# Performance work log

Hardware: AMD Instinct MI355X
Metric: run time of the kernel (lower is better)

Reference implementation:

```python
import jax, jax.numpy as jnp
import numpy as np

B, S, D, H = 512, 200, 512, 8
FF = 1024          # dim_feedforward == hidden_dim
EMB, HID, FIN = 128, 1024, 64
V = 100000
QK_SCALE, ATTN_CLIP, FFN_CLIP, QKV_CLIP = 0.05, 3.0, 2.0, 1.0
PAD = 0


def _ln(x, g, b, eps=1e-6):
    m = jnp.mean(x, -1, keepdims=True)
    v = jnp.mean((x - m) ** 2, -1, keepdims=True)
    return (x - m) / jnp.sqrt(v + eps) * g + b


def setup_inputs() -> dict:
    key = jax.random.key(0)
    ks = jax.random.split(key, 32)
    n = lambda i, shape, s=0.02: (s * jax.random.normal(ks[i], shape)).astype(jnp.float32)
    emb_table = n(0, (V, D)).at[PAD].set(0.0)  # padding row zeroed
    inp = {
        'item_seq': jax.random.randint(ks[20], (B, S), 0, V),
        'user_avg_ctr': jax.random.uniform(ks[21], (B,)),
        'user_total_interactions': jax.random.uniform(ks[22], (B,)),
        'age_price': jax.random.randint(ks[23], (B,), 0, 100),
        'gender_cate': jax.random.randint(ks[24], (B,), 0, 10),
        'cms_group_id': jax.random.randint(ks[25], (B,), 0, 13),
        'emb_table': emb_table,
        'in_proj_w': n(1, (3 * D, D)),
        'out_proj_w': n(2, (D, D)),
        'out_proj_b': jnp.zeros((D,), jnp.float32),
        'ln1_g': jnp.ones((D,), jnp.float32), 'ln1_b': jnp.zeros((D,), jnp.float32),
        'ln2_g': jnp.ones((D,), jnp.float32), 'ln2_b': jnp.zeros((D,), jnp.float32),
        'lin1_w': n(3, (FF, D)), 'lin1_b': jnp.zeros((FF,), jnp.float32),
        'lin2_w': n(4, (D, FF)), 'lin2_b': jnp.zeros((D,), jnp.float32),
        'age_tab': n(5, (100, EMB)), 'gender_tab': n(6, (10, EMB)), 'cms_tab': n(7, (13, EMB)),
        'ctr_w': n(8, (EMB, 1)), 'ctr_b': jnp.zeros((EMB,), jnp.float32),
        'ti_w': n(9, (EMB, 1)), 'ti_b': jnp.zeros((EMB,), jnp.float32),
        'mlp1_w': n(10, (HID, D + 5 * EMB)), 'mlp1_b': jnp.zeros((HID,), jnp.float32),
        'mlp2_w': n(11, (FIN, HID)), 'mlp2_b': jnp.zeros((FIN,), jnp.float32),
    }
    return inp


def reference(item_seq, user_avg_ctr, user_total_interactions, age_price, gender_cate,
              cms_group_id, emb_table, in_proj_w, out_proj_w, out_proj_b,
              ln1_g, ln1_b, ln2_g, ln2_b, lin1_w, lin1_b, lin2_w, lin2_b,
              age_tab, gender_tab, cms_tab, ctr_w, ctr_b, ti_w, ti_b,
              mlp1_w, mlp1_b, mlp2_w, mlp2_b):
    dk = D // H
    pad = item_seq == PAD  # [B,S] key padding mask
    x = jnp.clip(emb_table[item_seq] * 0.5, -1.0, 1.0)  # [B,S,D]

    # ---- custom self-attention block (no in_proj bias, heavy clamping) ----
    qw, kw, vw = in_proj_w[:D], in_proj_w[D:2 * D], in_proj_w[2 * D:]
    q = jnp.clip(x @ qw.T, -QKV_CLIP, QKV_CLIP)
    k = jnp.clip(x @ kw.T, -QKV_CLIP, QKV_CLIP)
    v = jnp.clip(x @ vw.T, -QKV_CLIP, QKV_CLIP)
    q = q.reshape(B, S, H, dk).transpose(0, 2, 1, 3)
    k = k.reshape(B, S, H, dk).transpose(0, 2, 1, 3)
    v = v.reshape(B, S, H, dk).transpose(0, 2, 1, 3)
    scores = jnp.einsum('bhqd,bhkd->bhqk', q, k) / (np.float32(np.sqrt(dk)) * QK_SCALE)
    scores = jnp.clip(scores, -ATTN_CLIP, ATTN_CLIP)
    scores = jnp.where(pad[:, None, None, :], -1e9, scores)
    w = jax.nn.softmax(scores, axis=-1)  # dropout is identity in eval
    x2 = jnp.einsum('bhqk,bhkd->bhqd', w, v).transpose(0, 2, 1, 3).reshape(B, S, D)
    x2 = jnp.clip(x2 @ out_proj_w.T + out_proj_b, -ATTN_CLIP, ATTN_CLIP)
    sa = _ln(x + x2, ln1_g, ln1_b)          # norm1 inside overridden _sa_block
    x = _ln(x + sa, ln1_g, ln1_b)           # base post-norm wraps norm1 again

    # ---- FFN block with clamps ----
    h = jax.nn.relu(jnp.clip(x @ lin1_w.T + lin1_b, -FFN_CLIP, FFN_CLIP))
    f2 = jnp.clip(h @ lin2_w.T + lin2_b, -FFN_CLIP, FFN_CLIP)
    ff = _ln(x + f2, ln2_g, ln2_b)          # norm2 inside overridden _ff_block
    x = _ln(x + ff, ln2_g, ln2_b)           # base wraps norm2 again

    seq_out = jnp.clip(x, -5.0, 5.0)
    m = (~pad).astype(seq_out.dtype)[:, :, None]
    seq_rep = jnp.clip((seq_out * m).sum(1) / (m.sum(1) + 1e-8), -5.0, 5.0)  # [B,D]

    ape = age_tab[age_price]
    ge = gender_tab[gender_cate]
    ce = cms_tab[cms_group_id]
    ctr = user_avg_ctr[:, None] @ ctr_w.T + ctr_b
    ti = user_total_interactions[:, None] @ ti_w.T + ti_b
    u = jnp.concatenate([seq_rep, ctr, ti, ape, ge, ce], axis=-1)  # [B, D+5*EMB]
    return jax.nn.relu(u @ mlp1_w.T + mlp1_b) @ mlp2_w.T + mlp2_b  # [B, FIN]
```

## Files before the change

kernel.cpp:

```cpp
#include <hip/hip_runtime.h>
#include <hip/hip_bf16.h>
#include <stdint.h>

typedef __attribute__((ext_vector_type(8))) short short8;
typedef __attribute__((ext_vector_type(4))) float f32x4;
typedef unsigned short u16;

#define MFMA16(a,b,c) __builtin_amdgcn_mfma_f32_16x16x32_bf16((a),(b),(c),0,0,0)

__device__ __forceinline__ u16 f2bf(float f) {
  unsigned int u = __float_as_uint(f);
  return (u16)((u + 0x7FFFu + ((u >> 16) & 1u)) >> 16);
}
__device__ __forceinline__ float bf2f(u16 h) {
  return __uint_as_float(((unsigned int)h) << 16);
}
__device__ __forceinline__ float clampf(float v, float lo, float hi) {
  return fminf(fmaxf(v, lo), hi);
}
__device__ __forceinline__ void gl2lds16(const u16* g, u16* l) {
  __builtin_amdgcn_global_load_lds(
      (const __attribute__((address_space(1))) unsigned int*)g,
      (__attribute__((address_space(3))) unsigned int*)(uintptr_t)l,
      16, 0, 0);
}

__global__ __launch_bounds__(256) void cvt_bf16_kernel(
    const float* __restrict__ src, u16* __restrict__ dst, int n) {
  for (int i = blockIdx.x*256 + threadIdx.x; i < n; i += gridDim.x*256)
    dst[i] = f2bf(src[i]);
}

__global__ __launch_bounds__(256) void embed_kernel(
    const int* __restrict__ iseq, const float* __restrict__ emb,
    u16* __restrict__ xb) {
  int gid = blockIdx.x*256 + threadIdx.x;
  int m = gid >> 7;
  int c = (gid & 127) * 4;
  int item = iseq[m];
  float4 e = *(const float4*)&emb[(size_t)item*512 + c];
  ushort4 hb;
  hb.x = f2bf(clampf(e.x*0.5f, -1.f, 1.f));
  hb.y = f2bf(clampf(e.y*0.5f, -1.f, 1.f));
  hb.z = f2bf(clampf(e.z*0.5f, -1.f, 1.f));
  hb.w = f2bf(clampf(e.w*0.5f, -1.f, 1.f));
  *(ushort4*)&xb[(size_t)m*512 + c] = hb;
}

__global__ __launch_bounds__(256) void cnt_kernel(
    const int* __restrict__ item_seq, float* __restrict__ cnt) {
  __shared__ int sred[4];
  int b = blockIdx.x, tid = threadIdx.x;
  int lane = tid & 63, wv = tid >> 6;
  int c = 0;
  if (tid < 200) c = (item_seq[b*200 + tid] != 0) ? 1 : 0;
  #pragma unroll
  for (int m = 1; m <= 32; m <<= 1) c += __shfl_xor(c, m);
  if (lane == 0) sred[wv] = c;
  __syncthreads();
  if (tid == 0) cnt[b] = (float)(sred[0]+sred[1]+sred[2]+sred[3]);
}

#define BAR() asm volatile("s_barrier" ::: "memory")
#define LGKM0() do { asm volatile("s_waitcnt lgkmcnt(0)" ::: "memory"); \
                     __builtin_amdgcn_sched_barrier(0); } while (0)
#define VM4() asm volatile("s_waitcnt vmcnt(4)" ::: "memory")
#define VM0() asm volatile("s_waitcnt vmcnt(0)" ::: "memory")

__device__ __forceinline__ void stage_half(const char* gsrc0, size_t rstride,
                                           u16* lhalf, int wv, int lane) {
  #pragma unroll
  for (int j = 0; j < 2; ++j) {
    const int o   = j*8192 + wv*1024 + lane*16;
    const int row = o >> 7;
    const int cb  = (o & 127) ^ ((row & 7) << 4);
    gl2lds16((const u16*)(gsrc0 + (size_t)row*rstride + cb),
             (u16*)((char*)lhalf + j*8192 + wv*1024));
  }
}

__device__ __forceinline__ short8 ldsfrag(const u16* slot, int row, int kb) {
  return *(const short8*)((const char*)slot + row*128 + (kb ^ ((row & 7) << 4)));
}

#define QUAD(AH, NB)                                                          \
  _Pragma("unroll")                                                           \
  for (int i = 0; i < 4; ++i)                                                 \
    _Pragma("unroll")                                                         \
    for (int nf = 0; nf < 2; ++nf)                                            \
      _Pragma("unroll")                                                       \
      for (int ks = 0; ks < 2; ++ks)                                          \
        acc[(AH)*4 + i][(NB)*2 + nf] =                                        \
            MFMA16(af[AH][i][ks], bf[nf][ks], acc[(AH)*4 + i][(NB)*2 + nf]);

#define RD_AF(H, SLOT)                                                        \
  _Pragma("unroll")                                                           \
  for (int i = 0; i < 4; ++i)                                                 \
    _Pragma("unroll")                                                         \
    for (int ks = 0; ks < 2; ++ks)                                            \
      af[H][i][ks] = ldsfrag((SLOT), wm*128 + (H)*64 + i*16 + r16, ks*64 + q4*16);

#define RD_BF(SLOT, OFF)                                                      \
  _Pragma("unroll")                                                           \
  for (int nf = 0; nf < 2; ++nf)                                              \
    _Pragma("unroll")                                                         \
    for (int ks = 0; ks < 2; ++ks)                                            \
      bf[nf][ks] = ldsfrag((SLOT), wn*64 + (OFF) + nf*16 + r16, ks*64 + q4*16);

template <int MODE>
__global__ __launch_bounds__(512, 2)
void gemm_bt(const u16* __restrict__ A, const u16* __restrict__ Bw,
             const float* __restrict__ bias, int K, int Nt, int swz,
             u16* __restrict__ outB, u16* __restrict__ QKV, long long projStride) {
  __shared__ __align__(16) u16 SH[65536];
  u16* const As0 = SH;
  u16* const As1 = SH + 16384;
  u16* const Bs0 = SH + 32768;
  u16* const Bs1 = SH + 49152;
  const int tid  = threadIdx.x;
  const int lane = tid & 63;
  const int wv   = tid >> 6;
  const int wm   = wv >> 2;
  const int wn   = wv & 3;
  const int id   = blockIdx.x;
  int mt, nt2;
  if (swz) { mt = (id / (8*Nt))*8 + (id & 7); nt2 = (id >> 3) % Nt; }
  else     { mt = id / Nt;                    nt2 = id % Nt; }
  const int m0 = mt * 256;
  const int n0 = nt2 * 256;
  const int KT = K >> 6;
  const int NI = KT >> 1;

  const char* Abase = (const char*)(A  + (size_t)m0*K);
  const char* Bbase = (const char*)(Bw + (size_t)n0*K);
  const size_t rs = (size_t)K * 2;

  const int r16 = lane & 15;
  const int q4  = lane >> 4;

  const f32x4 fz = {0.f, 0.f, 0.f, 0.f};
  f32x4 acc[8][4];
  #pragma unroll
  for (int i = 0; i < 8; ++i)
    #pragma unroll
    for (int j = 0; j < 4; ++j) acc[i][j] = fz;

  short8 af[2][4][2];
  short8 bf[2][2];

  stage_half(Abase,              rs, As0,             wv, lane);
  stage_half(Abase + 128*rs,     rs, As0 + 128*64,    wv, lane);
  stage_half(Bbase,              rs, Bs0,             wv, lane);
  stage_half(Bbase + 128*rs,     rs, Bs0 + 128*64,    wv, lane);
  stage_half(Abase + 128,        rs, As1,             wv, lane);
  stage_half(Abase + 128*rs + 128, rs, As1 + 128*64,  wv, lane);
  VM4();
  BAR();

  for (int it = 0; it < NI; ++it) {
    const int ta = it*2;
    const bool m2 = (ta + 2 < KT);
    const char* gBb  = Bbase + (size_t)(ta+1)*128;
    const char* gAa2 = Abase + (size_t)(ta+2)*128;
    const char* gBa2 = Bbase + (size_t)(ta+2)*128;
    const char* gAb1 = Abase + (size_t)(ta+3)*128;

    RD_AF(0, As0); RD_BF(Bs0, 0);
    asm volatile("s_waitcnt lgkmcnt(8)" ::: "memory");
    stage_half(gBb, rs, Bs1, wv, lane);
    BAR(); LGKM0();
    __builtin_amdgcn_s_setprio(1); QUAD(0, 0); __builtin_amdgcn_s_setprio(0);
    VM4(); BAR();

    RD_AF(1, As0);
    stage_half(gBb + 128*rs, rs, Bs1 + 128*64, wv, lane);
    BAR(); LGKM0();
    __builtin_amdgcn_s_setprio(1); QUAD(1, 0); __builtin_amdgcn_s_setprio(0);
    VM4(); BAR();

    RD_BF(Bs0, 32);
    if (m2) stage_half(gAa2, rs, As0, wv, lane);
    BAR(); LGKM0();
    __builtin_amdgcn_s_setprio(1); QUAD(1, 1); __builtin_amdgcn_s_setprio(0);
    VM4(); BAR();

    if (m2) stage_half(gAa2 + 128*rs, rs, As0 + 128*64, wv, lane);
    BAR();
    __builtin_amdgcn_s_setprio(1); QUAD(0, 1); __builtin_amdgcn_s_setprio(0);
    if (m2) { VM4(); } else { VM0(); }
    BAR();

    RD_AF(0, As1); RD_BF(Bs1, 0);
    asm volatile("s_waitcnt lgkmcnt(8)" ::: "memory");
    if (m2) stage_half(gBa2, rs, Bs0, wv, lane);
    BAR(); LGKM0();
    __builtin_amdgcn_s_setprio(1); QUAD(0, 0); __builtin_amdgcn_s_setprio(0);
    VM4(); BAR();

    RD_AF(1, As1);
    if (m2) stage_half(gBa2 + 128*rs, rs, Bs0 + 128*64, wv, lane);
    BAR(); LGKM0();
    __builtin_amdgcn_s_setprio(1); QUAD(1, 0); __builtin_amdgcn_s_setprio(0);
    VM4(); BAR();

    RD_BF(Bs1, 32);
    if (m2) stage_half(gAb1, rs, As1, wv, lane);
    BAR(); LGKM0();
    __builtin_amdgcn_s_setprio(1); QUAD(1, 1); __builtin_amdgcn_s_setprio(0);
    VM4(); BAR();

    if (m2) stage_half(gAb1 + 128*rs, rs, As1 + 128*64, wv, lane);
    BAR();
    __builtin_amdgcn_s_setprio(1); QUAD(0, 1); __builtin_amdgcn_s_setprio(0);
    VM4(); BAR();
  }

  {
    u16* const L = SH;
    const int LROW = 272;
    #pragma unroll
    for (int h = 0; h < 2; ++h) {
      if (h == 1) __syncthreads();
      if (wm == h) {
        #pragma unroll
        for (int nf = 0; nf < 4; ++nf) {
          const int col_l = wn*64 + nf*16 + r16;
          const float bvs = (MODE == 0) ? 0.f : bias[n0 + col_l];
          #pragma unroll
          for (int mi = 0; mi < 8; ++mi) {
            const int row_l = mi*16 + q4*4;
            #pragma unroll
            for (int r = 0; r < 4; ++r) {
              float v = acc[mi][nf][r];
              if (MODE == 0)      v = clampf(v, -1.f, 1.f);
              else if (MODE == 1) v = clampf(v + bvs, -3.f, 3.f);
              else if (MODE == 2) v = fmaxf(clampf(v + bvs, -2.f, 2.f), 0.f);
              else                v = clampf(v + bvs, -2.f, 2.f);
              L[(row_l + r)*LROW + col_l] = f2bf(v);
            }
          }
        }
      }
      __syncthreads();
      #pragma unroll
      for (int k = 0; k < 8; ++k) {
        const int ch   = wv*512 + k*64 + lane;
        const int row  = ch >> 5;
        const int colu = (ch & 31) * 8;
        short8 d = *(const short8*)&L[row*LROW + colu];
        const int rowg = m0 + h*128 + row;
        const int cg   = n0 + colu;
        if (MODE == 0) {
          const unsigned proj = (unsigned)cg >> 9;
          const unsigned hh   = ((unsigned)cg >> 6) & 7u;
          const unsigned dk   = (unsigned)cg & 63u;
          const int b = rowg / 200;
          const int s = rowg - b*200;
          *(short8*)&QKV[(size_t)proj*projStride + (size_t)hh*12800
                         + (size_t)b*102400 + (size_t)s*64 + dk] = d;
        } else {
          const int N = (MODE == 2) ? 1024 : 512;
          *(short8*)&outB[(size_t)rowg*N + cg] = d;
        }
      }
    }
  }
}

__global__ __launch_bounds__(512)
void attn_kernel(const u16* __restrict__ Q, const u16* __restrict__ K,
                 const u16* __restrict__ V, const int* __restrict__ iseq,
                 u16* __restrict__ x2b) {
  __shared__ __align__(16) u16 Ks[208*72];
  __shared__ __align__(16) u16 Vs[64*232];
  __shared__ __align__(16) u16 Ps[8][16*40];
  __shared__ float msk[208];

  const int tid = threadIdx.x, lane = tid & 63, wv = tid >> 6;
  const unsigned bid = blockIdx.x;
  const int h = bid & 7;
  const int b = bid >> 3;
  const size_t bh = (size_t)b*8 + h;
  const u16* Kg = K + bh*12800;
  const u16* Vg = V + bh*12800;
  const u16* Qg = Q + bh*12800;

  for (int c = tid; c < 3200; c += 512) {
    int row = c >> 4, q = c & 15;
    *(ushort4*)&Ks[row*72 + q*4] = *(const ushort4*)&Kg[row*64 + q*4];
  }
  {
    const int quad = wv*2 + (lane >> 5);
    const int sl   = lane & 31;
    #pragma unroll
    for (int it = 0; it < 7; ++it) {
      const int s = sl + it*32;
      if (s < 200) {
        ushort4 v4 = *(const ushort4*)&Vg[s*64 + quad*4];
        Vs[(quad*4+0)*232 + s] = v4.x;
        Vs[(quad*4+1)*232 + s] = v4.y;
        Vs[(quad*4+2)*232 + s] = v4.z;
        Vs[(quad*4+3)*232 + s] = v4.w;
      }
    }
  }
  for (int c = tid; c < 2048; c += 512) {
    int dk = c >> 5, s2 = 200 + (c & 31);
    Vs[dk*232 + s2] = 0;
  }
  for (int t = tid; t < 208; t += 512)
    msk[t] = (t < 200 && iseq[b*200 + t] != 0) ? 1.f : 0.f;
  __syncthreads();

  const int colk = lane & 15;
  const int fk8 = (lane >> 4) * 8;
  const int prow = (lane >> 4) * 4;
  const f32x4 fz = {0.f,0.f,0.f,0.f};

  for (int qb = 0; qb < 2; ++qb) {
    const int qrow = qb*128 + wv*16 + (lane & 15);
    const int qsrc = qrow < 200 ? qrow : 199;
    short8 qa0 = *(const short8*)&Qg[(size_t)qsrc*64 + fk8];
    short8 qa1 = *(const short8*)&Qg[(size_t)qsrc*64 + 32 + fk8];
    f32x4 oacc[4];
    #pragma unroll
    for (int nt = 0; nt < 4; ++nt) oacc[nt] = fz;
    float rs[4] = {0.f,0.f,0.f,0.f};

    for (int kt2 = 0; kt2 < 7; ++kt2) {
      #pragma unroll
      for (int half = 0; half < 2; ++half) {
        const int stile = kt2*2 + half;
        if (stile < 13) {
          const int key = stile*16 + colk;
          short8 kb0 = *(const short8*)&Ks[key*72 + fk8];
          short8 kb1 = *(const short8*)&Ks[key*72 + 32 + fk8];
          f32x4 sc = fz;
          __builtin_amdgcn_s_setprio(1);
          sc = MFMA16(qa0, kb0, sc);
          sc = MFMA16(qa1, kb1, sc);
          __builtin_amdgcn_s_setprio(0);
          const float mk = msk[key];
          #pragma unroll
          for (int r = 0; r < 4; ++r) {
            float p = __expf(clampf(sc[r]*2.5f, -3.f, 3.f)) * mk;
            rs[r] += p;
            Ps[wv][(prow + r)*40 + half*16 + colk] = f2bf(p);
          }
        } else {
          #pragma unroll
          for (int r = 0; r < 4; ++r)
            Ps[wv][(prow + r)*40 + half*16 + colk] = 0;
        }
      }
      asm volatile("s_waitcnt lgkmcnt(0)" ::: "memory");
      short8 pa = *(const short8*)&Ps[wv][(lane & 15)*40 + fk8];
      const int kb32 = kt2*32;
      __builtin_amdgcn_s_setprio(1);
      #pragma unroll
      for (int nt = 0; nt < 4; ++nt) {
        short8 vb = *(const short8*)&Vs[(nt*16 + colk)*232 + kb32 + fk8];
        oacc[nt] = MFMA16(pa, vb, oacc[nt]);
      }
      __builtin_amdgcn_s_setprio(0);
      asm volatile("s_waitcnt lgkmcnt(0)" ::: "memory");
    }

    #pragma unroll
    for (int m = 1; m <= 8; m <<= 1)
      #pragma unroll
      for (int r = 0; r < 4; ++r) rs[r] += __shfl_xor(rs[r], m);

    const int srow = qb*128 + wv*16 + prow;
    #pragma unroll
    for (int r = 0; r < 4; ++r) {
      const int s = srow + r;
      if (s < 200) {
        const float inv = rs[r] > 0.f ? 1.f/rs[r] : 0.f;
        const size_t base = ((size_t)b*200 + s)*512 + h*64;
        #pragma unroll
        for (int nt = 0; nt < 4; ++nt)
          x2b[base + nt*16 + colk] = f2bf(oacc[nt][r] * inv);
      }
    }
  }
}

__global__ __launch_bounds__(256)
void ln1_kernel(const u16* __restrict__ xb, const u16* __restrict__ x2b,
                const float* __restrict__ g, const float* __restrict__ bb,
                u16* __restrict__ xnb) {
  const int lane = threadIdx.x & 63, wv = threadIdx.x >> 6;
  const size_t t = (size_t)blockIdx.x*4 + wv;
  const int c0 = lane*4, c1 = 256 + lane*4;
  ushort4 xa = *(const ushort4*)&xb[t*512 + c0];
  ushort4 xc = *(const ushort4*)&xb[t*512 + c1];
  ushort4 ha = *(const ushort4*)&x2b[t*512 + c0];
  ushort4 hc = *(const ushort4*)&x2b[t*512 + c1];
  float xv[8] = {bf2f(xa.x),bf2f(xa.y),bf2f(xa.z),bf2f(xa.w),
                 bf2f(xc.x),bf2f(xc.y),bf2f(xc.z),bf2f(xc.w)};
  float tv[8] = {xv[0]+bf2f(ha.x), xv[1]+bf2f(ha.y), xv[2]+bf2f(ha.z), xv[3]+bf2f(ha.w),
                 xv[4]+bf2f(hc.x), xv[5]+bf2f(hc.y), xv[6]+bf2f(hc.z), xv[7]+bf2f(hc.w)};
  float s1 = 0.f, s2 = 0.f;
  #pragma unroll
  for (int i = 0; i < 8; ++i) { s1 += tv[i]; s2 += tv[i]*tv[i]; }
  #pragma unroll
  for (int m = 1; m <= 32; m <<= 1) { s1 += __shfl_xor(s1, m); s2 += __shfl_xor(s2, m); }
  float mean = s1*(1.f/512.f);
  float inv = 1.f/sqrtf(s2*(1.f/512.f) - mean*mean + 1e-6f);
  float4 ga = *(const float4*)(g + c0), gc = *(const float4*)(g + c1);
  float4 ba = *(const float4*)(bb + c0), bc = *(const float4*)(bb + c1);
  float gv[8] = {ga.x,ga.y,ga.z,ga.w, gc.x,gc.y,gc.z,gc.w};
  float bv[8] = {ba.x,ba.y,ba.z,ba.w, bc.x,bc.y,bc.z,bc.w};
  float uv[8]; float s3 = 0.f, s4 = 0.f;
  #pragma unroll
  for (int i = 0; i < 8; ++i) {
    float sa = (tv[i]-mean)*inv*gv[i] + bv[i];
    uv[i] = xv[i] + sa;
    s3 += uv[i]; s4 += uv[i]*uv[i];
  }
  #pragma unroll
  for (int m = 1; m <= 32; m <<= 1) { s3 += __shfl_xor(s3, m); s4 += __shfl_xor(s4, m); }
  float mean2 = s3*(1.f/512.f);
  float inv2 = 1.f/sqrtf(s4*(1.f/512.f) - mean2*mean2 + 1e-6f);
  ushort4 o0, o1;
  o0.x = f2bf((uv[0]-mean2)*inv2*gv[0] + bv[0]);
  o0.y = f2bf((uv[1]-mean2)*inv2*gv[1] + bv[1]);
  o0.z = f2bf((uv[2]-mean2)*inv2*gv[2] + bv[2]);
  o0.w = f2bf((uv[3]-mean2)*inv2*gv[3] + bv[3]);
  o1.x = f2bf((uv[4]-mean2)*inv2*gv[4] + bv[4]);
  o1.y = f2bf((uv[5]-mean2)*inv2*gv[5] + bv[5]);
  o1.z = f2bf((uv[6]-mean2)*inv2*gv[6] + bv[6]);
  o1.w = f2bf((uv[7]-mean2)*inv2*gv[7] + bv[7]);
  *(ushort4*)&xnb[t*512 + c0] = o0;
  *(ushort4*)&xnb[t*512 + c1] = o1;
}

__global__ __launch_bounds__(256)
void ln2_kernel(const u16* __restrict__ xnb, const u16* __restrict__ f2b,
                const float* __restrict__ g, const float* __restrict__ bb,
                const int* __restrict__ iseq, float* __restrict__ seq_acc) {
  const int tid = threadIdx.x, lane = tid & 63, wv = tid >> 6;
  const int q = blockIdx.x, bl = blockIdx.y;
  const int c8 = lane*8;
  float gv[8], bv[8];
  *(float4*)&gv[0] = *(const float4*)(g + c8);
  *(float4*)&gv[4] = *(const float4*)(g + c8 + 4);
  *(float4*)&bv[0] = *(const float4*)(bb + c8);
  *(float4*)&bv[4] = *(const float4*)(bb + c8 + 4);
  float acc[8] = {};
  for (int i = wv; i < 50; i += 4) {
    const int s = q*50 + i;
    const size_t row = (size_t)bl*200 + s;
    short8 xh = *(const short8*)&xnb[row*512 + c8];
    short8 yh = *(const short8*)&f2b[row*512 + c8];
    float xv[8], tv[8];
    #pragma unroll
    for (int j = 0; j < 8; ++j) {
      xv[j] = bf2f((u16)xh[j]);
      tv[j] = xv[j] + bf2f((u16)yh[j]);
    }
    float s1 = 0.f, s2 = 0.f;
    #pragma unroll
    for (int j = 0; j < 8; ++j) { s1 += tv[j]; s2 += tv[j]*tv[j]; }
    #pragma unroll
    for (int m = 1; m <= 32; m <<= 1) { s1 += __shfl_xor(s1,m); s2 += __shfl_xor(s2,m); }
    float mean = s1*(1.f/512.f);
    float inv = 1.f/sqrtf(s2*(1.f/512.f) - mean*mean + 1e-6f);
    float uv[8]; float s3 = 0.f, s4 = 0.f;
    #pragma unroll
    for (int j = 0; j < 8; ++j) {
      uv[j] = xv[j] + (tv[j]-mean)*inv*gv[j] + bv[j];
      s3 += uv[j]; s4 += uv[j]*uv[j];
    }
    #pragma unroll
    for (int m = 1; m <= 32; m <<= 1) { s3 += __shfl_xor(s3,m); s4 += __shfl_xor(s4,m); }
    float mean2 = s3*(1.f/512.f);
    float inv2 = 1.f/sqrtf(s4*(1.f/512.f) - mean2*mean2 + 1e-6f);
    if (iseq[row] != 0) {
      #pragma unroll
      for (int j = 0; j < 8; ++j)
        acc[j] += clampf((uv[j]-mean2)*inv2*gv[j] + bv[j], -5.f, 5.f);
    }
  }
  float* dst = &seq_acc[(((size_t)bl*4 + q)*4 + wv)*512 + c8];
  *(float4*)&dst[0] = *(float4*)&acc[0];
  *(float4*)&dst[4] = *(float4*)&acc[4];
}

__global__ __launch_bounds__(256)
void build_u_kernel(const float* __restrict__ seq_acc, const float* __restrict__ cnt,
                    const float* __restrict__ uac, const float* __restrict__ uti,
                    const int* __restrict__ age, const int* __restrict__ gen,
                    const int* __restrict__ cms,
                    const float* __restrict__ age_tab, const float* __restrict__ gen_tab,
                    const float* __restrict__ cms_tab,
                    const float* __restrict__ ctr_w, const float* __restrict__ ctr_b,
                    const float* __restrict__ ti_w, const float* __restrict__ ti_b,
                    float* __restrict__ u) {
  const int b = blockIdx.x;
  for (int j = threadIdx.x; j < 1152; j += 256) {
    float v;
    if (j < 512) {
      float ssum = 0.f;
      #pragma unroll
      for (int p = 0; p < 16; ++p) ssum += seq_acc[((size_t)b*16 + p)*512 + j];
      v = clampf(ssum / (cnt[b] + 1e-8f), -5.f, 5.f);
    }
    else if (j < 640)  { int e = j-512;  v = uac[b]*ctr_w[e] + ctr_b[e]; }
    else if (j < 768)  { int e = j-640;  v = uti[b]*ti_w[e] + ti_b[e]; }
    else if (j < 896)  { int e = j-768;  v = age_tab[age[b]*128 + e]; }
    else if (j < 1024) { int e = j-896;  v = gen_tab[gen[b]*128 + e]; }
    else               { int e = j-1024; v = cms_tab[cms[b]*128 + e]; }
    u[(size_t)b*1152 + j] = v;
  }
}

__global__ __launch_bounds__(256)
void mlp1_kernel(const float* __restrict__ u, const float* __restrict__ w,
                 const float* __restrict__ bias, float* __restrict__ h1) {
  __shared__ __align__(16) float As[64][36];
  __shared__ __align__(16) float Wt[32][68];
  const int tid = threadIdx.x;
  const int m0 = blockIdx.x*64, n0 = blockIdx.y*64;
  const int tm = tid >> 4, tn = tid & 15;
  float acc[4][4] = {};
  for (int k0 = 0; k0 < 1152; k0 += 32) {
    for (int c = tid; c < 512; c += 256) {
      int row = c >> 3, q = c & 7;
      *(float4*)&As[row][q*4] = *(const float4*)&u[(size_t)(m0+row)*1152 + k0 + q*4];
      float4 wv4 = *(const float4*)&w[(size_t)(n0+row)*1152 + k0 + q*4];
      Wt[q*4+0][row] = wv4.x; Wt[q*4+1][row] = wv4.y;
      Wt[q*4+2][row] = wv4.z; Wt[q*4+3][row] = wv4.w;
    }
    __syncthreads();
    #pragma unroll
    for (int kk = 0; kk < 32; ++kk) {
      float av[4], bw[4];
      #pragma unroll
      for (int i = 0; i < 4; ++i) av[i] = As[tm*4+i][kk];
      #pragma unroll
      for (int j = 0; j < 4; ++j) bw[j] = Wt[kk][tn*4+j];
      #pragma unroll
      for (int i = 0; i < 4; ++i)
        #pragma unroll
        for (int j = 0; j < 4; ++j) acc[i][j] += av[i]*bw[j];
    }
    __syncthreads();
  }
  #pragma unroll
  for (int i = 0; i < 4; ++i)
    #pragma unroll
    for (int j = 0; j < 4; ++j) {
      int n = n0 + tn*4 + j;
      h1[(size_t)(m0 + tm*4 + i)*1024 + n] = fmaxf(acc[i][j] + bias[n], 0.f);
    }
}

__global__ __launch_bounds__(256)
void mlp2_kernel(const float* __restrict__ h1, const float* __restrict__ w,
                 const float* __restrict__ bias, float* __restrict__ out) {
  const int tid = threadIdx.x;
  const int m = blockIdx.x*4 + (tid >> 6);
  const int n = tid & 63;
  const float4* hr = (const float4*)(h1 + (size_t)m*1024);
  const float4* wr = (const float4*)(w + (size_t)n*1024);
  float acc = 0.f;
  for (int k4 = 0; k4 < 256; ++k4) {
    float4 a = hr[k4], bw = wr[k4];
    acc += a.x*bw.x + a.y*bw.y + a.z*bw.z + a.w*bw.w;
  }
  out[(size_t)m*64 + n] = acc + bias[n];
}

extern "C" void kernel_launch(void* const* d_in, const int* in_sizes, int n_in,
                              void* d_out, int out_size, void* d_ws, size_t ws_size,
                              hipStream_t stream) {
  (void)in_sizes; (void)n_in; (void)out_size;
  const int*   item_seq   = (const int*)d_in[0];
  const float* uac        = (const float*)d_in[1];
  const float* uti        = (const float*)d_in[2];
  const int*   age        = (const int*)d_in[3];
  const int*   gen        = (const int*)d_in[4];
  const int*   cms        = (const int*)d_in[5];
  const float* emb        = (const float*)d_in[6];
  const float* in_proj_w  = (const float*)d_in[7];
  const float* out_proj_w = (const float*)d_in[8];
  const float* out_proj_b = (const float*)d_in[9];
  const float* ln1_g = (const float*)d_in[10];
  const float* ln1_b = (const float*)d_in[11];
  const float* ln2_g = (const float*)d_in[12];
  const float* ln2_b = (const float*)d_in[13];
  const float* lin1_w = (const float*)d_in[14];
  const float* lin1_b = (const float*)d_in[15];
  const float* lin2_w = (const float*)d_in[16];
  const float* lin2_b = (const float*)d_in[17];
  const float* age_tab = (const float*)d_in[18];
  const float* gen_tab = (const float*)d_in[19];
  const float* cms_tab = (const float*)d_in[20];
  const float* ctr_w = (const float*)d_in[21];
  const float* ctr_b = (const float*)d_in[22];
  const float* ti_w  = (const float*)d_in[23];
  const float* ti_b  = (const float*)d_in[24];
  const float* mlp1_w = (const float*)d_in[25];
  const float* mlp1_b = (const float*)d_in[26];
  const float* mlp2_w = (const float*)d_in[27];
  const float* mlp2_b = (const float*)d_in[28];

  const long long TAILB = 25430016LL;
  int CB = 32;
  if      ((long long)ws_size >= 512LL*1024000 + TAILB) CB = 512;
  else if ((long long)ws_size >= 128LL*1024000 + TAILB) CB = 128;
  else if ((long long)ws_size >=  64LL*1024000 + TAILB) CB = 64;
  const long long R = (long long)CB * 204800;

  char* ws = (char*)d_ws;
  u16* xb   = (u16*)(ws);
  u16* x2b  = (u16*)(ws + R);
  u16* Qb   = (u16*)(ws + 2*R);
  u16* Kb   = (u16*)(ws + 3*R);
  u16* Vrb  = (u16*)(ws + 4*R);
  u16* x2o  = Qb;
  u16* xnb  = Kb;
  u16* f2b  = Vrb;
  u16* hbuf = (u16*)(ws);
  char* tail = ws + 5*R;
  float* seq_acc = (float*)(tail);
  float* cnt     = (float*)(tail + 16777216);
  float* u       = (float*)(tail + 16779264);
  float* h1      = (float*)(tail + 19138560);
  u16*   wqkv    = (u16*)(tail + 21235712);
  u16*   wout    = (u16*)(tail + 22808576);
  u16*   wl1     = (u16*)(tail + 23332864);
  u16*   wl2     = (u16*)(tail + 24381440);

  cvt_bf16_kernel<<<768, 256, 0, stream>>>(in_proj_w, wqkv, 1536*512);
  cvt_bf16_kernel<<<256, 256, 0, stream>>>(out_proj_w, wout, 512*512);
  cvt_bf16_kernel<<<512, 256, 0, stream>>>(lin1_w, wl1, 1024*512);
  cvt_bf16_kernel<<<512, 256, 0, stream>>>(lin2_w, wl2, 512*1024);
  cnt_kernel<<<512, 256, 0, stream>>>(item_seq, cnt);

  const int nch = 512 / CB;
  const int Mc  = CB * 200;
  const int Mt  = Mc / 256;
  const int swz = (Mt % 8 == 0) ? 1 : 0;
  const long long projStride = (long long)CB * 102400;
  for (int ch = 0; ch < nch; ++ch) {
    const int* iseq = item_seq + (size_t)ch*CB*200;
    embed_kernel<<<Mc/2, 256, 0, stream>>>(iseq, emb, xb);
    gemm_bt<0><<<Mt*6, 512, 0, stream>>>(xb, wqkv, nullptr, 512, 6, swz,
                                         nullptr, Qb, projStride);
    attn_kernel<<<CB*8, 512, 0, stream>>>(Qb, Kb, Vrb, iseq, x2b);
    gemm_bt<1><<<Mt*2, 512, 0, stream>>>(x2b, wout, out_proj_b, 512, 2, swz,
                                         x2o, nullptr, 0);
    ln1_kernel<<<Mc/4, 256, 0, stream>>>(xb, x2o, ln1_g, ln1_b, xnb);
    gemm_bt<2><<<Mt*4, 512, 0, stream>>>(xnb, wl1, lin1_b, 512, 4, swz,
                                         hbuf, nullptr, 0);
    gemm_bt<3><<<Mt*2, 512, 0, stream>>>(hbuf, wl2, lin2_b, 1024, 2, swz,
                                         f2b, nullptr, 0);
    ln2_kernel<<<dim3(4, CB), 256, 0, stream>>>(xnb, f2b, ln2_g, ln2_b, iseq,
                                                seq_acc + (size_t)ch*CB*8192);
  }

  build_u_kernel<<<512, 256, 0, stream>>>(seq_acc, cnt, uac, uti, age, gen, cms,
                                          age_tab, gen_tab, cms_tab,
                                          ctr_w, ctr_b, ti_w, ti_b, u);
  mlp1_kernel<<<dim3(8, 16), 256, 0, stream>>>(u, mlp1_w, mlp1_b, h1);
  mlp2_kernel<<<128, 256, 0, stream>>>(h1, mlp2_w, mlp2_b, (float*)d_out);
}
```

Measured before the change: 1.381 ms.

## Load GEMM B fragments directly from global into registers, keep only A in LDS

The GEMM main loop no longer stages the weight (B) tile through LDS. Each wave loads its B fragments straight from global memory into double-buffered registers one k-step ahead, while A stays double-buffered in LDS. The loop is restructured into a two-phase k-step lambda with new vmcnt waits, and shared memory is cut roughly in half. This saves LDS traffic and space, but the B loads are uncoalesced per-lane 16-byte reads, other waves in the block re-read the same B data, and register pressure rises.

```diff
diff --git a/kernel.cpp b/kernel.cpp
--- a/kernel.cpp
+++ b/kernel.cpp
@@ -64,8 +64,7 @@
 #define BAR() asm volatile("s_barrier" ::: "memory")
 #define LGKM0() do { asm volatile("s_waitcnt lgkmcnt(0)" ::: "memory"); \
                      __builtin_amdgcn_sched_barrier(0); } while (0)
-#define VM4() asm volatile("s_waitcnt vmcnt(4)" ::: "memory")
-#define VM0() asm volatile("s_waitcnt vmcnt(0)" ::: "memory")
+#define VMW(N) asm volatile("s_waitcnt vmcnt(" #N ")" ::: "memory")
 
 __device__ __forceinline__ void stage_half(const char* gsrc0, size_t rstride,
                                            u16* lhalf, int wv, int lane) {
@@ -83,40 +82,14 @@
   return *(const short8*)((const char*)slot + row*128 + (kb ^ ((row & 7) << 4)));
 }
 
-#define QUAD(AH, NB)                                                          \
-  _Pragma("unroll")                                                           \
-  for (int i = 0; i < 4; ++i)                                                 \
-    _Pragma("unroll")                                                         \
-    for (int nf = 0; nf < 2; ++nf)                                            \
-      _Pragma("unroll")                                                       \
-      for (int ks = 0; ks < 2; ++ks)                                          \
-        acc[(AH)*4 + i][(NB)*2 + nf] =                                        \
-            MFMA16(af[AH][i][ks], bf[nf][ks], acc[(AH)*4 + i][(NB)*2 + nf]);
-
-#define RD_AF(H, SLOT)                                                        \
-  _Pragma("unroll")                                                           \
-  for (int i = 0; i < 4; ++i)                                                 \
-    _Pragma("unroll")                                                         \
-    for (int ks = 0; ks < 2; ++ks)                                            \
-      af[H][i][ks] = ldsfrag((SLOT), wm*128 + (H)*64 + i*16 + r16, ks*64 + q4*16);
-
-#define RD_BF(SLOT, OFF)                                                      \
-  _Pragma("unroll")                                                           \
-  for (int nf = 0; nf < 2; ++nf)                                              \
-    _Pragma("unroll")                                                         \
-    for (int ks = 0; ks < 2; ++ks)                                            \
-      bf[nf][ks] = ldsfrag((SLOT), wn*64 + (OFF) + nf*16 + r16, ks*64 + q4*16);
-
 template <int MODE>
 __global__ __launch_bounds__(512, 2)
 void gemm_bt(const u16* __restrict__ A, const u16* __restrict__ Bw,
              const float* __restrict__ bias, int K, int Nt, int swz,
              u16* __restrict__ outB, u16* __restrict__ QKV, long long projStride) {
-  __shared__ __align__(16) u16 SH[65536];
+  __shared__ __align__(16) u16 SH[34816];
   u16* const As0 = SH;
   u16* const As1 = SH + 16384;
-  u16* const Bs0 = SH + 32768;
-  u16* const Bs1 = SH + 49152;
   const int tid  = threadIdx.x;
   const int lane = tid & 63;
   const int wv   = tid >> 6;
@@ -129,7 +102,6 @@
   const int m0 = mt * 256;
   const int n0 = nt2 * 256;
   const int KT = K >> 6;
-  const int NI = KT >> 1;
 
   const char* Abase = (const char*)(A  + (size_t)m0*K);
   const char* Bbase = (const char*)(Bw + (size_t)n0*K);
@@ -137,6 +109,7 @@
 
   const int r16 = lane & 15;
   const int q4  = lane >> 4;
+  const size_t browB = (size_t)(wn*64 + r16)*rs + q4*16;
 
   const f32x4 fz = {0.f, 0.f, 0.f, 0.f};
   f32x4 acc[8][4];
@@ -145,74 +118,76 @@
     #pragma unroll
     for (int j = 0; j < 4; ++j) acc[i][j] = fz;
 
-  short8 af[2][4][2];
-  short8 bf[2][2];
-
-  stage_half(Abase,              rs, As0,             wv, lane);
-  stage_half(Abase + 128*rs,     rs, As0 + 128*64,    wv, lane);
-  stage_half(Bbase,              rs, Bs0,             wv, lane);
-  stage_half(Bbase + 128*rs,     rs, Bs0 + 128*64,    wv, lane);
-  stage_half(Abase + 128,        rs, As1,             wv, lane);
-  stage_half(Abase + 128*rs + 128, rs, As1 + 128*64,  wv, lane);
-  VM4();
+  short8 af[4][2];
+  short8 bfA[4][2], bfB[4][2];
+
+  #pragma unroll
+  for (int nf = 0; nf < 4; ++nf)
+    #pragma unroll
+    for (int ks = 0; ks < 2; ++ks)
+      bfA[nf][ks] = *(const short8*)(Bbase + browB + (size_t)nf*16*rs + ks*64);
+  stage_half(Abase,              rs, As0,            wv, lane);
+  stage_half(Abase + 128*rs,     rs, As0 + 128*64,   wv, lane);
+  stage_half(Abase + 128,        rs, As1,            wv, lane);
+  VMW(2);
   BAR();
 
+  auto kstep = [&](int t, u16* Acur, u16* Aoth,
+                   short8 (&bfC)[4][2], short8 (&bfN)[4][2]) {
+    const bool l1 = (t + 1 < KT);
+    const bool l2 = (t + 2 < KT);
+    const char* Bg1 = Bbase + (size_t)(t+1)*128;
+    const char* Ag1 = Abase + (size_t)(t+1)*128;
+    const char* Ag2 = Abase + (size_t)(t+2)*128;
+    if (l1) {
+      #pragma unroll
+      for (int nf = 0; nf < 4; ++nf)
+        #pragma unroll
+        for (int ks = 0; ks < 2; ++ks)
+          bfN[nf][ks] = *(const short8*)(Bg1 + browB + (size_t)nf*16*rs + ks*64);
+    }
+    #pragma unroll
+    for (int i = 0; i < 4; ++i)
+      #pragma unroll
+      for (int ks = 0; ks < 2; ++ks)
+        af[i][ks] = ldsfrag(Acur, wm*128 + i*16 + r16, ks*64 + q4*16);
+    if (l1) stage_half(Ag1 + 128*rs, rs, Aoth + 128*64, wv, lane);
+    BAR(); LGKM0();
+    __builtin_amdgcn_s_setprio(1);
+    #pragma unroll
+    for (int i = 0; i < 4; ++i)
+      #pragma unroll
+      for (int nf = 0; nf < 4; ++nf)
+        #pragma unroll
+        for (int ks = 0; ks < 2; ++ks)
+          acc[i][nf] = MFMA16(af[i][ks], bfC[nf][ks], acc[i][nf]);
+    __builtin_amdgcn_s_setprio(0);
+    if (l1) { VMW(12); } else { VMW(0); }
+    BAR();
+    #pragma unroll
+    for (int i = 0; i < 4; ++i)
+      #pragma unroll
+      for (int ks = 0; ks < 2; ++ks)
+        af[i][ks] = ldsfrag(Acur, wm*128 + 64 + i*16 + r16, ks*64 + q4*16);
+    if (l2) stage_half(Ag2, rs, Acur, wv, lane);
+    BAR(); LGKM0();
+    __builtin_amdgcn_s_setprio(1);
+    #pragma unroll
+    for (int i = 0; i < 4; ++i)
+      #pragma unroll
+      for (int nf = 0; nf < 4; ++nf)
+        #pragma unroll
+        for (int ks = 0; ks < 2; ++ks)
+          acc[4+i][nf] = MFMA16(af[i][ks], bfC[nf][ks], acc[4+i][nf]);
+    __builtin_amdgcn_s_setprio(0);
+    if (l2) { VMW(12); } else if (l1) { VMW(10); }
+    BAR();
+  };
+
+  const int NI = KT >> 1;
   for (int it = 0; it < NI; ++it) {
-    const int ta = it*2;
-    const bool m2 = (ta + 2 < KT);
-    const char* gBb  = Bbase + (size_t)(ta+1)*128;
-    const char* gAa2 = Abase + (size_t)(ta+2)*128;
-    const char* gBa2 = Bbase + (size_t)(ta+2)*128;
-    const char* gAb1 = Abase + (size_t)(ta+3)*128;
-
-    RD_AF(0, As0); RD_BF(Bs0, 0);
-    asm volatile("s_waitcnt lgkmcnt(8)" ::: "memory");
-    stage_half(gBb, rs, Bs1, wv, lane);
-    BAR(); LGKM0();
-    __builtin_amdgcn_s_setprio(1); QUAD(0, 0); __builtin_amdgcn_s_setprio(0);
-    VM4(); BAR();
-
-    RD_AF(1, As0);
-    stage_half(gBb + 128*rs, rs, Bs1 + 128*64, wv, lane);
-    BAR(); LGKM0();
-    __builtin_amdgcn_s_setprio(1); QUAD(1, 0); __builtin_amdgcn_s_setprio(0);
-    VM4(); BAR();
-
-    RD_BF(Bs0, 32);
-    if (m2) stage_half(gAa2, rs, As0, wv, lane);
-    BAR(); LGKM0();
-    __builtin_amdgcn_s_setprio(1); QUAD(1, 1); __builtin_amdgcn_s_setprio(0);
-    VM4(); BAR();
-
-    if (m2) stage_half(gAa2 + 128*rs, rs, As0 + 128*64, wv, lane);
-    BAR();
-    __builtin_amdgcn_s_setprio(1); QUAD(0, 1); __builtin_amdgcn_s_setprio(0);
-    if (m2) { VM4(); } else { VM0(); }
-    BAR();
-
-    RD_AF(0, As1); RD_BF(Bs1, 0);
-    asm volatile("s_waitcnt lgkmcnt(8)" ::: "memory");
-    if (m2) stage_half(gBa2, rs, Bs0, wv, lane);
-    BAR(); LGKM0();
-    __builtin_amdgcn_s_setprio(1); QUAD(0, 0); __builtin_amdgcn_s_setprio(0);
-    VM4(); BAR();
-
-    RD_AF(1, As1);
-    if (m2) stage_half(gBa2 + 128*rs, rs, Bs0 + 128*64, wv, lane);
-    BAR(); LGKM0();
-    __builtin_amdgcn_s_setprio(1); QUAD(1, 0); __builtin_amdgcn_s_setprio(0);
-    VM4(); BAR();
-
-    RD_BF(Bs1, 32);
-    if (m2) stage_half(gAb1, rs, As1, wv, lane);
-    BAR(); LGKM0();
-    __builtin_amdgcn_s_setprio(1); QUAD(1, 1); __builtin_amdgcn_s_setprio(0);
-    VM4(); BAR();
-
-    if (m2) stage_half(gAb1 + 128*rs, rs, As1 + 128*64, wv, lane);
-    BAR();
-    __builtin_amdgcn_s_setprio(1); QUAD(0, 1); __builtin_amdgcn_s_setprio(0);
-    VM4(); BAR();
+    kstep(it*2,     As0, As1, bfA, bfB);
+    kstep(it*2 + 1, As1, As0, bfB, bfA);
   }
 
   {
```

Result: slower. 1.649 ms (+19.3%).
